# Optimization experiments

Measured on AMD Instinct MI355X. Metric: run time of the kernel, lower is better.

## Reference

```python
import jax, jax.numpy as jnp
import numpy as np

B, L, D, H, DH, M = 2, 2048, 512, 8, 2048, 128  # batch, seq, d_model, heads, d_hidden, max_rel_pos
HD = D // H
EPS = 1e-5


def _ln(x, w, b):
    mu = jnp.mean(x, axis=-1, keepdims=True)
    var = jnp.mean((x - mu) ** 2, axis=-1, keepdims=True)
    return (x - mu) * jax.lax.rsqrt(var + EPS) * w + b


def setup_inputs() -> dict:
    key = jax.random.key(0)
    ks = jax.random.split(key, 8)
    s = 0.02  # init std for weights
    return {
        "x": jax.random.normal(ks[0], (B, L, D), jnp.float32),
        "ln1_w": jnp.ones((D,), jnp.float32),
        "ln1_b": jnp.zeros((D,), jnp.float32),
        "qkv_w": jax.random.normal(ks[1], (D, 3 * D), jnp.float32) * s,
        "qkv_b": jnp.zeros((3 * D,), jnp.float32),
        "out_w": jax.random.normal(ks[2], (D, D), jnp.float32) * s,
        "out_b": jnp.zeros((D,), jnp.float32),
        "rel_bias": jax.random.normal(ks[3], (H, 2 * M - 1), jnp.float32) * s,
        "gamma1": 1e-4 * jnp.ones((D,), jnp.float32),
        "ln2_w": jnp.ones((D,), jnp.float32),
        "ln2_b": jnp.zeros((D,), jnp.float32),
        "ffn_in_w": jax.random.normal(ks[4], (D, 2 * DH), jnp.float32) * s,
        "ffn_in_b": jnp.zeros((2 * DH,), jnp.float32),
        "ffn_out_w": jax.random.normal(ks[5], (DH, D), jnp.float32) * s,
        "ffn_out_b": jnp.zeros((D,), jnp.float32),
        "gamma2": 1e-4 * jnp.ones((D,), jnp.float32),
    }


def _forward(x, ln1_w, ln1_b, qkv_w, qkv_b, out_w, out_b, rel_bias, gamma1,
             ln2_w, ln2_b, ffn_in_w, ffn_in_b, ffn_out_w, ffn_out_b, gamma2):
    b, l, d = x.shape
    # --- PreNorm attention with T5-style relative position bias ---
    h = _ln(x, ln1_w, ln1_b)
    qkv = h @ qkv_w + qkv_b                           # [B, L, 3D]
    q, k, v = jnp.split(qkv, 3, axis=-1)
    q = q.reshape(b, l, H, HD)
    k = k.reshape(b, l, H, HD)
    v = v.reshape(b, l, H, HD)
    scale = 1.0 / jnp.sqrt(jnp.asarray(HD, x.dtype))
    scores = jnp.einsum("bqhd,bkhd->bhqk", q, k) * scale   # [B, H, L, L]
    # relative position bias: clip(i - j) indexed into learned table
    ctx = jnp.arange(l)[:, None] - jnp.arange(l)[None, :]
    ctx = jnp.clip(ctx, -(M - 1), M - 1) + (M - 1)          # [L, L] in [0, 2M-2]
    rel = rel_bias[:, ctx]                                  # [H, L, L]
    scores = scores + rel[None]
    attn = jax.nn.softmax(scores, axis=-1)
    o = jnp.einsum("bhqk,bkhd->bqhd", attn, v).reshape(b, l, d)
    o = o @ out_w + out_b
    x = x + o * gamma1                                      # LayerScale residual
    # --- PreNorm GEGLU FFN ---
    h2 = _ln(x, ln2_w, ln2_b)
    ab = h2 @ ffn_in_w + ffn_in_b                           # [B, L, 2*DH]
    a, bgate = jnp.split(ab, 2, axis=-1)
    f = jax.nn.gelu(bgate, approximate=False) * a
    f = f @ ffn_out_w + ffn_out_b
    x = x + f * gamma2
    return x, attn


def reference(x, ln1_w, ln1_b, qkv_w, qkv_b, out_w, out_b, rel_bias, gamma1,
              ln2_w, ln2_b, ffn_in_w, ffn_in_b, ffn_out_w, ffn_out_b, gamma2):
    return _forward(x, ln1_w, ln1_b, qkv_w, qkv_b, out_w, out_b, rel_bias, gamma1,
                    ln2_w, ln2_b, ffn_in_w, ffn_in_b, ffn_out_w, ffn_out_b, gamma2)
```

## Files before the change

### kernel.cpp

```cpp
#include <hip/hip_runtime.h>
#include <math.h>

typedef __attribute__((ext_vector_type(4))) float f32x4;
typedef __attribute__((ext_vector_type(8))) short bf16x8;
typedef __attribute__((ext_vector_type(4))) short s16x4;

#if __has_builtin(__builtin_amdgcn_exp2f)
#define EXP2(x) __builtin_amdgcn_exp2f(x)
#else
#define EXP2(x) exp2f(x)
#endif

__device__ __forceinline__ unsigned short f2bf(float f) {
  union { float f; unsigned u; } v; v.f = f;
  return (unsigned short)((v.u + 0x7fffu + ((v.u >> 16) & 1u)) >> 16);
}

__global__ void ln_kernel(const float* __restrict__ in, const float* __restrict__ w,
                          const float* __restrict__ b, unsigned short* __restrict__ out) {
  __shared__ float sh[4];
  const int t = threadIdx.x;
  const float* p = in + (size_t)blockIdx.x * 512;
  float a0 = p[t], a1 = p[t + 256];
  float s = a0 + a1;
#pragma unroll
  for (int o = 32; o; o >>= 1) s += __shfl_down(s, o);
  if ((t & 63) == 0) sh[t >> 6] = s;
  __syncthreads();
  s = sh[0] + sh[1] + sh[2] + sh[3];
  float mu = s * (1.0f / 512.0f);
  float d0 = a0 - mu, d1 = a1 - mu;
  float q = d0 * d0 + d1 * d1;
  __syncthreads();
#pragma unroll
  for (int o = 32; o; o >>= 1) q += __shfl_down(q, o);
  if ((t & 63) == 0) sh[t >> 6] = q;
  __syncthreads();
  q = sh[0] + sh[1] + sh[2] + sh[3];
  float rstd = rsqrtf(q * (1.0f / 512.0f) + 1e-5f);
  unsigned short* po = out + (size_t)blockIdx.x * 512;
  po[t]       = f2bf(d0 * rstd * w[t] + b[t]);
  po[t + 256] = f2bf(d1 * rstd * w[t + 256] + b[t + 256]);
}

__global__ void transpose_w(const float* __restrict__ in, unsigned short* __restrict__ out,
                            int ldi, int ldo, long ibs, long obs) {
  __shared__ float tile[32][33];
  const float* ip = in + (long)blockIdx.z * ibs;
  unsigned short* op = out + (long)blockIdx.z * obs;
  const int tx = threadIdx.x & 31;
  const int ty = threadIdx.x >> 5;
  const int n0 = blockIdx.x * 32, k0 = blockIdx.y * 32;
#pragma unroll
  for (int i = 0; i < 4; ++i)
    tile[ty + i * 8][tx] = ip[(size_t)(k0 + ty + i * 8) * ldi + n0 + tx];
  __syncthreads();
#pragma unroll
  for (int i = 0; i < 4; ++i)
    op[(size_t)(n0 + ty + i * 8) * ldo + k0 + tx] = f2bf(tile[tx][ty + i * 8]);
}

template <int WM, int WN, int TM, int TN, int EPI>
__global__ __launch_bounds__(256) void gemm_bb(
    const unsigned short* __restrict__ A, const unsigned short* __restrict__ Bt,
    float* __restrict__ C, unsigned short* __restrict__ Cbf,
    int K, int lda, int ldb, int ldc,
    const float* __restrict__ bias, const float* __restrict__ resid,
    const float* __restrict__ gamma) {
  constexpr int BM = WM * TM * 16;
  constexpr int BN = WN * TN * 16;
  __shared__ short As[BM * 32];
  __shared__ short Bs[BN * 32];

  const int tid = threadIdx.x;
  const int m0 = blockIdx.y * BM, n0 = blockIdx.x * BN;
  const int w = tid >> 6, lane = tid & 63;
  const int wm = w / WN, wn = w % WN;
  const int lrow = lane & 15, lq = lane >> 4;

  f32x4 acc[TM][TN];
#pragma unroll
  for (int i = 0; i < TM; ++i)
#pragma unroll
    for (int j = 0; j < TN; ++j) acc[i][j] = (f32x4){0.f, 0.f, 0.f, 0.f};

  for (int k0 = 0; k0 < K; k0 += 32) {
    __syncthreads();
#pragma unroll
    for (int it = 0; it < BM / 64; ++it) {
      int c = it * 256 + tid;
      int row = c >> 2, col = (c & 3) << 3;
      *(bf16x8*)(As + row * 32 + col) =
          *(const bf16x8*)(A + (size_t)(m0 + row) * lda + k0 + col);
    }
#pragma unroll
    for (int it = 0; it < BN / 64; ++it) {
      int c = it * 256 + tid;
      int row = c >> 2, col = (c & 3) << 3;
      *(bf16x8*)(Bs + row * 32 + col) =
          *(const bf16x8*)(Bt + (size_t)(n0 + row) * ldb + k0 + col);
    }
    __syncthreads();

    bf16x8 af[TM], bf[TN];
#pragma unroll
    for (int mi = 0; mi < TM; ++mi)
      af[mi] = *(const bf16x8*)(As + (wm * TM * 16 + mi * 16 + lrow) * 32 + lq * 8);
#pragma unroll
    for (int nj = 0; nj < TN; ++nj)
      bf[nj] = *(const bf16x8*)(Bs + (wn * TN * 16 + nj * 16 + lrow) * 32 + lq * 8);
#pragma unroll
    for (int mi = 0; mi < TM; ++mi)
#pragma unroll
      for (int nj = 0; nj < TN; ++nj)
        acc[mi][nj] = __builtin_amdgcn_mfma_f32_16x16x32_bf16(af[mi], bf[nj], acc[mi][nj], 0, 0, 0);
  }

#pragma unroll
  for (int mi = 0; mi < TM; ++mi) {
#pragma unroll
    for (int nj = 0; nj < TN; ++nj) {
      int gm0 = m0 + wm * TM * 16 + mi * 16 + lq * 4;
      int gn = n0 + wn * TN * 16 + nj * 16 + lrow;
#pragma unroll
      for (int r = 0; r < 4; ++r) {
        int gm = gm0 + r;
        size_t idx = (size_t)gm * ldc + gn;
        float v = acc[mi][nj][r];
        if constexpr (EPI == 0) {
          C[idx] = v + bias[gn];
        } else if constexpr (EPI == 4) {
          float u = v + bias[gn];
          if (gn < 1024)
            Cbf[idx] = f2bf(gn < 512 ? u * 0.18033688011112042f : u);
          else
            C[idx] = u;
        } else {
          C[idx] = resid[idx] + (v + bias[gn]) * gamma[gn];
        }
      }
    }
  }
}

__global__ __launch_bounds__(256) void ffn1_gate_kernel(
    const unsigned short* __restrict__ A, const unsigned short* __restrict__ Bt,
    unsigned short* __restrict__ F, const float* __restrict__ bias) {
  __shared__ short As[128 * 32];
  __shared__ short Bs[64 * 32];
  __shared__ short Bs2[64 * 32];

  const int tid = threadIdx.x;
  const int n0 = blockIdx.x * 64, m0 = blockIdx.y * 128;
  const int w = tid >> 6, lane = tid & 63;
  const int wm = w >> 1, wn = w & 1;
  const int lrow = lane & 15, lq = lane >> 4;

  f32x4 acca[4][2], accb[4][2];
#pragma unroll
  for (int i = 0; i < 4; ++i)
#pragma unroll
    for (int j = 0; j < 2; ++j) {
      acca[i][j] = (f32x4){0.f, 0.f, 0.f, 0.f};
      accb[i][j] = (f32x4){0.f, 0.f, 0.f, 0.f};
    }

  for (int k0 = 0; k0 < 512; k0 += 32) {
    __syncthreads();
#pragma unroll
    for (int it = 0; it < 2; ++it) {
      int c = it * 256 + tid;
      int row = c >> 2, col = (c & 3) << 3;
      *(bf16x8*)(As + row * 32 + col) =
          *(const bf16x8*)(A + (size_t)(m0 + row) * 512 + k0 + col);
    }
    {
      int c = tid;
      int row = c >> 2, col = (c & 3) << 3;
      *(bf16x8*)(Bs + row * 32 + col) =
          *(const bf16x8*)(Bt + (size_t)(n0 + row) * 512 + k0 + col);
      *(bf16x8*)(Bs2 + row * 32 + col) =
          *(const bf16x8*)(Bt + (size_t)(2048 + n0 + row) * 512 + k0 + col);
    }
    __syncthreads();

    bf16x8 af[4], ba[2], bb[2];
#pragma unroll
    for (int mi = 0; mi < 4; ++mi)
      af[mi] = *(const bf16x8*)(As + (wm * 64 + mi * 16 + lrow) * 32 + lq * 8);
#pragma unroll
    for (int nj = 0; nj < 2; ++nj) {
      ba[nj] = *(const bf16x8*)(Bs + (wn * 32 + nj * 16 + lrow) * 32 + lq * 8);
      bb[nj] = *(const bf16x8*)(Bs2 + (wn * 32 + nj * 16 + lrow) * 32 + lq * 8);
    }
#pragma unroll
    for (int mi = 0; mi < 4; ++mi)
#pragma unroll
      for (int nj = 0; nj < 2; ++nj) {
        acca[mi][nj] = __builtin_amdgcn_mfma_f32_16x16x32_bf16(af[mi], ba[nj], acca[mi][nj], 0, 0, 0);
        accb[mi][nj] = __builtin_amdgcn_mfma_f32_16x16x32_bf16(af[mi], bb[nj], accb[mi][nj], 0, 0, 0);
      }
  }

#pragma unroll
  for (int mi = 0; mi < 4; ++mi)
#pragma unroll
    for (int nj = 0; nj < 2; ++nj) {
      int gm0 = m0 + wm * 64 + mi * 16 + lq * 4;
      int gn = n0 + wn * 32 + nj * 16 + lrow;
#pragma unroll
      for (int r = 0; r < 4; ++r) {
        float a = acca[mi][nj][r] + bias[gn];
        float bg = accb[mi][nj][r] + bias[2048 + gn];
        float g = 0.5f * bg * (1.0f + erff(bg * 0.70710678118654752f));
        F[(size_t)(gm0 + r) * 2048 + gn] = f2bf(g * a);
      }
    }
}

__global__ __launch_bounds__(256, 4) void attn_fused(
    const unsigned short* __restrict__ qkvbf, const unsigned short* __restrict__ vt,
    const float* __restrict__ rel, float* __restrict__ attn, unsigned short* __restrict__ o) {
  __shared__ __align__(16) float p_f32[4 * 16 * 64];
  __shared__ float erel[256];
  __shared__ float rsum[32];
  __shared__ float rinv[32];

  const int tid = threadIdx.x;
  const int flat = blockIdx.y * 64 + blockIdx.x;
  const int swz = (flat & 7) * 128 + (flat >> 3);
  const int bh = swz >> 6;
  const int m0 = (swz & 63) * 32;
  const int b = bh >> 3, h = bh & 7;

  const int w = tid >> 6, lane = tid & 63;
  const int wm = w >> 1, wn = w & 1;
  const int lrow = lane & 15, lq = lane >> 4;

  const unsigned short* qb = qkvbf + (size_t)(b * 2048) * 1536 + h * 64;
  const unsigned short* kb = qb + 512;
  const unsigned short* vb = vt + (size_t)bh * 64 * 2048;
  float* ab = attn + (size_t)bh * 2048 * 2048;
  const float* relh = rel + h * 255;

  if (tid < 32) rsum[tid] = 0.f;
  if (tid < 255) erel[tid] = __expf(relh[tid]);

  bf16x8 qf[2];
#pragma unroll
  for (int c = 0; c < 2; ++c)
    qf[c] = *(const bf16x8*)(qb + (size_t)(m0 + wm * 16 + lrow) * 1536 + c * 32 + lq * 8);

  const unsigned short* krow = kb + (size_t)(wn * 64 + lrow) * 1536 + lq * 8;
  const unsigned short* vrow = vb + (size_t)lrow * 2048 + wn * 64 + lq * 8;

  __syncthreads();

  float psum[4] = {0.f, 0.f, 0.f, 0.f};
  const int dbase = (m0 + wm * 16 + lq * 4) - (wn * 64 + lrow);
  for (int t = 0; t < 16; ++t) {
    const int kt0 = t * 128;
    f32x4 acc[4];
#pragma unroll
    for (int nj = 0; nj < 4; ++nj) acc[nj] = (f32x4){0.f, 0.f, 0.f, 0.f};
#pragma unroll
    for (int c = 0; c < 2; ++c) {
      bf16x8 kf[4];
#pragma unroll
      for (int nj = 0; nj < 4; ++nj)
        kf[nj] = *(const bf16x8*)(krow + (size_t)(kt0 + nj * 16) * 1536 + c * 32);
#pragma unroll
      for (int nj = 0; nj < 4; ++nj)
        acc[nj] = __builtin_amdgcn_mfma_f32_16x16x32_bf16(qf[c], kf[nj], acc[nj], 0, 0, 0);
    }
    const int Dt = m0 - kt0;
    if (Dt >= 256 || Dt <= -160) {
      float ec = erel[Dt >= 256 ? 254 : 0];
#pragma unroll
      for (int r = 0; r < 4; ++r) {
        float s = 0.f;
#pragma unroll
        for (int nj = 0; nj < 4; ++nj) s += EXP2(acc[nj][r]);
        psum[r] += ec * s;
      }
    } else {
#pragma unroll
      for (int nj = 0; nj < 4; ++nj) {
        int d0 = dbase - kt0 - nj * 16;
#pragma unroll
        for (int r = 0; r < 4; ++r) {
          int d = d0 + r;
          d = d < -127 ? -127 : (d > 127 ? 127 : d);
          psum[r] += EXP2(acc[nj][r]) * erel[d + 127];
        }
      }
    }
  }
#pragma unroll
  for (int off = 1; off < 16; off <<= 1)
#pragma unroll
    for (int r = 0; r < 4; ++r) psum[r] += __shfl_xor(psum[r], off);
  if (lrow == 0) {
#pragma unroll
    for (int r = 0; r < 4; ++r) atomicAdd(&rsum[wm * 16 + lq * 4 + r], psum[r]);
  }
  __syncthreads();
  if (tid < 32) rinv[tid] = 1.0f / rsum[tid];
  __syncthreads();
  float rv[4];
#pragma unroll
  for (int r = 0; r < 4; ++r) rv[r] = rinv[wm * 16 + lq * 4 + r];

  f32x4 oacc[4];
#pragma unroll
  for (int nj = 0; nj < 4; ++nj) oacc[nj] = (f32x4){0.f, 0.f, 0.f, 0.f};
  float* pw = p_f32 + w * (16 * 64);

  const int wsw = lq << 4;
  const int rsw = ((lrow >> 2) & 3) << 4;

  for (int t = 0; t < 16; ++t) {
    const int kt0 = t * 128;
    f32x4 acc[4];
#pragma unroll
    for (int nj = 0; nj < 4; ++nj) acc[nj] = (f32x4){0.f, 0.f, 0.f, 0.f};
#pragma unroll
    for (int c = 0; c < 2; ++c) {
      bf16x8 kf[4];
#pragma unroll
      for (int nj = 0; nj < 4; ++nj)
        kf[nj] = *(const bf16x8*)(krow + (size_t)(kt0 + nj * 16) * 1536 + c * 32);
#pragma unroll
      for (int nj = 0; nj < 4; ++nj)
        acc[nj] = __builtin_amdgcn_mfma_f32_16x16x32_bf16(qf[c], kf[nj], acc[nj], 0, 0, 0);
    }

    const int Dt = m0 - kt0;
    if (Dt >= 256 || Dt <= -160) {
      float ec = erel[Dt >= 256 ? 254 : 0];
#pragma unroll
      for (int r = 0; r < 4; ++r) {
        float fr = ec * rv[r];
        int prow = lq * 4 + r;
#pragma unroll
        for (int nj = 0; nj < 4; ++nj) {
          float e = EXP2(acc[nj][r]) * fr;
          pw[prow * 64 + ((nj * 16 + lrow) ^ wsw)] = e;
        }
      }
    } else {
#pragma unroll
      for (int r = 0; r < 4; ++r) {
        int prow = lq * 4 + r;
        int d0 = dbase - kt0 + r;
#pragma unroll
        for (int nj = 0; nj < 4; ++nj) {
          int d = d0 - nj * 16;
          d = d < -127 ? -127 : (d > 127 ? 127 : d);
          float e = EXP2(acc[nj][r]) * (erel[d + 127] * rv[r]);
          pw[prow * 64 + ((nj * 16 + lrow) ^ wsw)] = e;
        }
      }
    }

#pragma unroll
    for (int it = 0; it < 4; ++it) {
      int rr = lq * 4 + it;
      f32x4 vv = *(const f32x4*)(pw + rr * 64 + ((lrow * 4) ^ wsw));
      __builtin_nontemporal_store(
          vv, (f32x4*)(ab + (size_t)(m0 + wm * 16 + rr) * 2048 + kt0 + wn * 64 + lrow * 4));
    }

#pragma unroll
    for (int c2 = 0; c2 < 2; ++c2) {
      const float* pp = pw + lrow * 64 + ((c2 * 32 + lq * 8) ^ rsw);
      f32x4 pa = *(const f32x4*)pp;
      f32x4 pb = *(const f32x4*)(pp + 4);
      bf16x8 ap = {(short)f2bf(pa[0]), (short)f2bf(pa[1]), (short)f2bf(pa[2]), (short)f2bf(pa[3]),
                   (short)f2bf(pb[0]), (short)f2bf(pb[1]), (short)f2bf(pb[2]), (short)f2bf(pb[3])};
      bf16x8 bv[4];
#pragma unroll
      for (int nj = 0; nj < 4; ++nj)
        bv[nj] = *(const bf16x8*)(vrow + (size_t)(nj * 16) * 2048 + kt0 + c2 * 32);
#pragma unroll
      for (int nj = 0; nj < 4; ++nj)
        oacc[nj] = __builtin_amdgcn_mfma_f32_16x16x32_bf16(ap, bv[nj], oacc[nj], 0, 0, 0);
    }
  }

  __syncthreads();
  float* osc = p_f32;
  if (wn == 0) {
#pragma unroll
    for (int nj = 0; nj < 4; ++nj)
#pragma unroll
      for (int r = 0; r < 4; ++r)
        osc[(wm * 16 + lq * 4 + r) * 64 + nj * 16 + lrow] = oacc[nj][r];
  }
  __syncthreads();
  if (wn == 1) {
#pragma unroll
    for (int nj = 0; nj < 4; ++nj)
#pragma unroll
      for (int r = 0; r < 4; ++r) {
        int rr = m0 + wm * 16 + lq * 4 + r;
        float v = oacc[nj][r] + osc[(wm * 16 + lq * 4 + r) * 64 + nj * 16 + lrow];
        o[(size_t)(b * 2048 + rr) * 512 + h * 64 + nj * 16 + lrow] = f2bf(v);
      }
  }
}

extern "C" void kernel_launch(void* const* d_in, const int* in_sizes, int n_in,
                              void* d_out, int out_size, void* d_ws, size_t ws_size,
                              hipStream_t stream) {
  (void)in_sizes; (void)n_in; (void)out_size; (void)ws_size;
  const float* x        = (const float*)d_in[0];
  const float* ln1_w    = (const float*)d_in[1];
  const float* ln1_b    = (const float*)d_in[2];
  const float* qkv_w    = (const float*)d_in[3];
  const float* qkv_b    = (const float*)d_in[4];
  const float* out_w    = (const float*)d_in[5];
  const float* out_b    = (const float*)d_in[6];
  const float* rel_bias = (const float*)d_in[7];
  const float* gamma1   = (const float*)d_in[8];
  const float* ln2_w    = (const float*)d_in[9];
  const float* ln2_b    = (const float*)d_in[10];
  const float* ffn_in_w = (const float*)d_in[11];
  const float* ffn_in_b = (const float*)d_in[12];
  const float* ffn_out_w  = (const float*)d_in[13];
  const float* ffn_out_b  = (const float*)d_in[14];
  const float* gamma2   = (const float*)d_in[15];

  float* x_out = (float*)d_out;
  float* attn  = x_out + (size_t)2 * 2048 * 512;

  float* ws  = (float*)d_ws;
  float* qkv = ws;
  float* x1  = qkv + 6291456;
  unsigned short* h_bf  = (unsigned short*)(x1 + 2097152);
  unsigned short* o_bf  = h_bf + 2097152;
  unsigned short* f_bf  = o_bf + 2097152;
  unsigned short* qkvbf = f_bf;
  unsigned short* bt_qkv  = f_bf + 8388608;
  unsigned short* bt_out  = bt_qkv + 786432;
  unsigned short* bt_ffn1 = bt_out + 262144;
  unsigned short* bt_ffn2 = bt_ffn1 + 2097152;
  unsigned short* vt      = bt_ffn2 + 1048576;

  transpose_w<<<dim3(48, 16, 1), 256, 0, stream>>>(qkv_w,     bt_qkv,  1536, 512,  0, 0);
  transpose_w<<<dim3(16, 16, 1), 256, 0, stream>>>(out_w,     bt_out,  512,  512,  0, 0);
  transpose_w<<<dim3(128, 16, 1), 256, 0, stream>>>(ffn_in_w, bt_ffn1, 4096, 512,  0, 0);
  transpose_w<<<dim3(16, 64, 1), 256, 0, stream>>>(ffn_out_w, bt_ffn2, 512,  2048, 0, 0);

  ln_kernel<<<4096, 256, 0, stream>>>(x, ln1_w, ln1_b, h_bf);

  gemm_bb<2, 2, 4, 2, 4><<<dim3(24, 32, 1), 256, 0, stream>>>(
      h_bf, bt_qkv, qkv, qkvbf, 512, 512, 512, 1536, qkv_b, nullptr, nullptr);

  transpose_w<<<dim3(2, 64, 8), 256, 0, stream>>>(
      qkv + 1024, vt, 1536, 2048, 64, (long)64 * 2048);
  transpose_w<<<dim3(2, 64, 8), 256, 0, stream>>>(
      qkv + (size_t)2048 * 1536 + 1024, vt + (size_t)8 * 64 * 2048, 1536, 2048, 64,
      (long)64 * 2048);

  attn_fused<<<dim3(64, 16, 1), 256, 0, stream>>>(qkvbf, vt, rel_bias, attn, o_bf);

  gemm_bb<2, 2, 4, 2, 3><<<dim3(8, 32, 1), 256, 0, stream>>>(
      o_bf, bt_out, x1, nullptr, 512, 512, 512, 512, out_b, x, gamma1);

  ln_kernel<<<4096, 256, 0, stream>>>(x1, ln2_w, ln2_b, h_bf);

  ffn1_gate_kernel<<<dim3(32, 32, 1), 256, 0, stream>>>(h_bf, bt_ffn1, f_bf, ffn_in_b);

  gemm_bb<2, 2, 4, 2, 3><<<dim3(8, 32, 1), 256, 0, stream>>>(
      f_bf, bt_ffn2, x_out, nullptr, 2048, 2048, 2048, 512, ffn_out_b, x1, gamma2);
}
```

Before: 572.1 us.

## Fuse V transpose into QKV GEMM, shrink attention tile, deepen GEMM K-step

The QKV GEMM epilogue now writes V straight to the transposed bf16 layout, which removes the fp32 qkv buffer and the two V transpose launches. The four weight transposes become a single launch. The GEMM and FFN1 kernels step K by 64 with padded LDS rows to cut syncs and bank conflicts. The out-proj and FFN2 GEMMs use smaller M tiles for more blocks. Attention now uses 16-row query tiles with four waves splitting keys and higher occupancy, at the cost of re-reading K/V more often and an extra cross-wave reduction.

After: 583.7 us. +2.0%, slower.

```diff
diff --git a/kernel.cpp b/kernel.cpp
--- a/kernel.cpp
+++ b/kernel.cpp
@@ -43,34 +43,41 @@
   po[t + 256] = f2bf(d1 * rstd * w[t + 256] + b[t + 256]);
 }
 
-__global__ void transpose_w(const float* __restrict__ in, unsigned short* __restrict__ out,
-                            int ldi, int ldo, long ibs, long obs) {
+__global__ void transpose_all(const float* __restrict__ w0, unsigned short* __restrict__ o0,
+                              const float* __restrict__ w1, unsigned short* __restrict__ o1,
+                              const float* __restrict__ w2, unsigned short* __restrict__ o2,
+                              const float* __restrict__ w3, unsigned short* __restrict__ o3) {
   __shared__ float tile[32][33];
-  const float* ip = in + (long)blockIdx.z * ibs;
-  unsigned short* op = out + (long)blockIdx.z * obs;
+  int idx = blockIdx.x;
+  const float* in; unsigned short* out; int ldi, ldo, nx;
+  if (idx < 768)        { in = w0; out = o0; ldi = 1536; ldo = 512;  nx = 48; }
+  else if (idx < 1024)  { idx -= 768;  in = w1; out = o1; ldi = 512;  ldo = 512;  nx = 16; }
+  else if (idx < 3072)  { idx -= 1024; in = w2; out = o2; ldi = 4096; ldo = 512;  nx = 128; }
+  else                  { idx -= 3072; in = w3; out = o3; ldi = 512;  ldo = 2048; nx = 16; }
   const int tx = threadIdx.x & 31;
   const int ty = threadIdx.x >> 5;
-  const int n0 = blockIdx.x * 32, k0 = blockIdx.y * 32;
+  const int n0 = (idx % nx) * 32, k0 = (idx / nx) * 32;
 #pragma unroll
   for (int i = 0; i < 4; ++i)
-    tile[ty + i * 8][tx] = ip[(size_t)(k0 + ty + i * 8) * ldi + n0 + tx];
+    tile[ty + i * 8][tx] = in[(size_t)(k0 + ty + i * 8) * ldi + n0 + tx];
   __syncthreads();
 #pragma unroll
   for (int i = 0; i < 4; ++i)
-    op[(size_t)(n0 + ty + i * 8) * ldo + k0 + tx] = f2bf(tile[tx][ty + i * 8]);
+    out[(size_t)(n0 + ty + i * 8) * ldo + k0 + tx] = f2bf(tile[tx][ty + i * 8]);
 }
 
 template <int WM, int WN, int TM, int TN, int EPI>
 __global__ __launch_bounds__(256) void gemm_bb(
     const unsigned short* __restrict__ A, const unsigned short* __restrict__ Bt,
-    float* __restrict__ C, unsigned short* __restrict__ Cbf,
+    float* __restrict__ C, unsigned short* __restrict__ Cbf, unsigned short* __restrict__ Vt,
     int K, int lda, int ldb, int ldc,
     const float* __restrict__ bias, const float* __restrict__ resid,
     const float* __restrict__ gamma) {
   constexpr int BM = WM * TM * 16;
   constexpr int BN = WN * TN * 16;
-  __shared__ short As[BM * 32];
-  __shared__ short Bs[BN * 32];
+  constexpr int LDS_STRIDE = 72;
+  __shared__ short As[BM * LDS_STRIDE];
+  __shared__ short Bs[BN * LDS_STRIDE];
 
   const int tid = threadIdx.x;
   const int m0 = blockIdx.y * BM, n0 = blockIdx.x * BN;
@@ -84,36 +91,42 @@
 #pragma unroll
     for (int j = 0; j < TN; ++j) acc[i][j] = (f32x4){0.f, 0.f, 0.f, 0.f};
 
-  for (int k0 = 0; k0 < K; k0 += 32) {
+  for (int k0 = 0; k0 < K; k0 += 64) {
     __syncthreads();
 #pragma unroll
-    for (int it = 0; it < BM / 64; ++it) {
+    for (int it = 0; it < BM / 32; ++it) {
       int c = it * 256 + tid;
-      int row = c >> 2, col = (c & 3) << 3;
-      *(bf16x8*)(As + row * 32 + col) =
+      int row = c >> 3, col = (c & 7) << 3;
+      *(bf16x8*)(As + row * LDS_STRIDE + col) =
           *(const bf16x8*)(A + (size_t)(m0 + row) * lda + k0 + col);
     }
 #pragma unroll
-    for (int it = 0; it < BN / 64; ++it) {
+    for (int it = 0; it < BN / 32; ++it) {
       int c = it * 256 + tid;
-      int row = c >> 2, col = (c & 3) << 3;
-      *(bf16x8*)(Bs + row * 32 + col) =
+      int row = c >> 3, col = (c & 7) << 3;
+      *(bf16x8*)(Bs + row * LDS_STRIDE + col) =
           *(const bf16x8*)(Bt + (size_t)(n0 + row) * ldb + k0 + col);
     }
     __syncthreads();
 
-    bf16x8 af[TM], bf[TN];
+    bf16x8 af[TM][2], bf[TN][2];
 #pragma unroll
     for (int mi = 0; mi < TM; ++mi)
-      af[mi] = *(const bf16x8*)(As + (wm * TM * 16 + mi * 16 + lrow) * 32 + lq * 8);
+#pragma unroll
+      for (int c = 0; c < 2; ++c)
+        af[mi][c] = *(const bf16x8*)(As + (wm * TM * 16 + mi * 16 + lrow) * LDS_STRIDE + c * 32 + lq * 8);
 #pragma unroll
     for (int nj = 0; nj < TN; ++nj)
-      bf[nj] = *(const bf16x8*)(Bs + (wn * TN * 16 + nj * 16 + lrow) * 32 + lq * 8);
+#pragma unroll
+      for (int c = 0; c < 2; ++c)
+        bf[nj][c] = *(const bf16x8*)(Bs + (wn * TN * 16 + nj * 16 + lrow) * LDS_STRIDE + c * 32 + lq * 8);
 #pragma unroll
     for (int mi = 0; mi < TM; ++mi)
 #pragma unroll
       for (int nj = 0; nj < TN; ++nj)
-        acc[mi][nj] = __builtin_amdgcn_mfma_f32_16x16x32_bf16(af[mi], bf[nj], acc[mi][nj], 0, 0, 0);
+#pragma unroll
+        for (int c = 0; c < 2; ++c)
+          acc[mi][nj] = __builtin_amdgcn_mfma_f32_16x16x32_bf16(af[mi][c], bf[nj][c], acc[mi][nj], 0, 0, 0);
   }
 
 #pragma unroll
@@ -122,6 +135,17 @@
     for (int nj = 0; nj < TN; ++nj) {
       int gm0 = m0 + wm * TM * 16 + mi * 16 + lq * 4;
       int gn = n0 + wn * TN * 16 + nj * 16 + lrow;
+      if constexpr (EPI == 4) {
+        if (gn >= 1024) {
+          int h = (gn - 1024) >> 6, dd = (gn - 1024) & 63;
+          int bb = gm0 >> 11, l0 = gm0 & 2047;
+          float bs = bias[gn];
+          s16x4 r4 = {(short)f2bf(acc[mi][nj][0] + bs), (short)f2bf(acc[mi][nj][1] + bs),
+                      (short)f2bf(acc[mi][nj][2] + bs), (short)f2bf(acc[mi][nj][3] + bs)};
+          *(s16x4*)(Vt + ((size_t)(bb * 8 + h) * 64 + dd) * 2048 + l0) = r4;
+          continue;
+        }
+      }
 #pragma unroll
       for (int r = 0; r < 4; ++r) {
         int gm = gm0 + r;
@@ -131,10 +155,7 @@
           C[idx] = v + bias[gn];
         } else if constexpr (EPI == 4) {
           float u = v + bias[gn];
-          if (gn < 1024)
-            Cbf[idx] = f2bf(gn < 512 ? u * 0.18033688011112042f : u);
-          else
-            C[idx] = u;
+          Cbf[idx] = f2bf(gn < 512 ? u * 0.18033688011112042f : u);
         } else {
           C[idx] = resid[idx] + (v + bias[gn]) * gamma[gn];
         }
@@ -146,9 +167,10 @@
 __global__ __launch_bounds__(256) void ffn1_gate_kernel(
     const unsigned short* __restrict__ A, const unsigned short* __restrict__ Bt,
     unsigned short* __restrict__ F, const float* __restrict__ bias) {
-  __shared__ short As[128 * 32];
-  __shared__ short Bs[64 * 32];
-  __shared__ short Bs2[64 * 32];
+  constexpr int LDS_STRIDE = 72;
+  __shared__ short As[128 * LDS_STRIDE];
+  __shared__ short Bs[64 * LDS_STRIDE];
+  __shared__ short Bs2[64 * LDS_STRIDE];
 
   const int tid = threadIdx.x;
   const int n0 = blockIdx.x * 64, m0 = blockIdx.y * 128;
@@ -165,41 +187,48 @@
       accb[i][j] = (f32x4){0.f, 0.f, 0.f, 0.f};
     }
 
-  for (int k0 = 0; k0 < 512; k0 += 32) {
+  for (int k0 = 0; k0 < 512; k0 += 64) {
     __syncthreads();
+#pragma unroll
+    for (int it = 0; it < 4; ++it) {
+      int c = it * 256 + tid;
+      int row = c >> 3, col = (c & 7) << 3;
+      *(bf16x8*)(As + row * LDS_STRIDE + col) =
+          *(const bf16x8*)(A + (size_t)(m0 + row) * 512 + k0 + col);
+    }
 #pragma unroll
     for (int it = 0; it < 2; ++it) {
       int c = it * 256 + tid;
-      int row = c >> 2, col = (c & 3) << 3;
-      *(bf16x8*)(As + row * 32 + col) =
-          *(const bf16x8*)(A + (size_t)(m0 + row) * 512 + k0 + col);
-    }
-    {
-      int c = tid;
-      int row = c >> 2, col = (c & 3) << 3;
-      *(bf16x8*)(Bs + row * 32 + col) =
+      int row = c >> 3, col = (c & 7) << 3;
+      *(bf16x8*)(Bs + row * LDS_STRIDE + col) =
           *(const bf16x8*)(Bt + (size_t)(n0 + row) * 512 + k0 + col);
-      *(bf16x8*)(Bs2 + row * 32 + col) =
+      *(bf16x8*)(Bs2 + row * LDS_STRIDE + col) =
           *(const bf16x8*)(Bt + (size_t)(2048 + n0 + row) * 512 + k0 + col);
     }
     __syncthreads();
 
-    bf16x8 af[4], ba[2], bb[2];
+    bf16x8 af[4][2], ba[2][2], bb[2][2];
 #pragma unroll
     for (int mi = 0; mi < 4; ++mi)
-      af[mi] = *(const bf16x8*)(As + (wm * 64 + mi * 16 + lrow) * 32 + lq * 8);
-#pragma unroll
-    for (int nj = 0; nj < 2; ++nj) {
-      ba[nj] = *(const bf16x8*)(Bs + (wn * 32 + nj * 16 + lrow) * 32 + lq * 8);
-      bb[nj] = *(const bf16x8*)(Bs2 + (wn * 32 + nj * 16 + lrow) * 32 + lq * 8);
-    }
+#pragma unroll
+      for (int c = 0; c < 2; ++c)
+        af[mi][c] = *(const bf16x8*)(As + (wm * 64 + mi * 16 + lrow) * LDS_STRIDE + c * 32 + lq * 8);
+#pragma unroll
+    for (int nj = 0; nj < 2; ++nj)
+#pragma unroll
+      for (int c = 0; c < 2; ++c) {
+        ba[nj][c] = *(const bf16x8*)(Bs + (wn * 32 + nj * 16 + lrow) * LDS_STRIDE + c * 32 + lq * 8);
+        bb[nj][c] = *(const bf16x8*)(Bs2 + (wn * 32 + nj * 16 + lrow) * LDS_STRIDE + c * 32 + lq * 8);
+      }
 #pragma unroll
     for (int mi = 0; mi < 4; ++mi)
 #pragma unroll
-      for (int nj = 0; nj < 2; ++nj) {
-        acca[mi][nj] = __builtin_amdgcn_mfma_f32_16x16x32_bf16(af[mi], ba[nj], acca[mi][nj], 0, 0, 0);
-        accb[mi][nj] = __builtin_amdgcn_mfma_f32_16x16x32_bf16(af[mi], bb[nj], accb[mi][nj], 0, 0, 0);
-      }
+      for (int nj = 0; nj < 2; ++nj)
+#pragma unroll
+        for (int c = 0; c < 2; ++c) {
+          acca[mi][nj] = __builtin_amdgcn_mfma_f32_16x16x32_bf16(af[mi][c], ba[nj][c], acca[mi][nj], 0, 0, 0);
+          accb[mi][nj] = __builtin_amdgcn_mfma_f32_16x16x32_bf16(af[mi][c], bb[nj][c], accb[mi][nj], 0, 0, 0);
+        }
   }
 
 #pragma unroll
@@ -218,23 +247,22 @@
     }
 }
 
-__global__ __launch_bounds__(256, 4) void attn_fused(
+__global__ __launch_bounds__(256, 8) void attn_fused(
     const unsigned short* __restrict__ qkvbf, const unsigned short* __restrict__ vt,
     const float* __restrict__ rel, float* __restrict__ attn, unsigned short* __restrict__ o) {
-  __shared__ __align__(16) float p_f32[4 * 16 * 64];
+  __shared__ __align__(16) float scr[3072];
   __shared__ float erel[256];
-  __shared__ float rsum[32];
-  __shared__ float rinv[32];
+  __shared__ float rsum[16];
+  __shared__ float rinv[16];
 
   const int tid = threadIdx.x;
-  const int flat = blockIdx.y * 64 + blockIdx.x;
-  const int swz = (flat & 7) * 128 + (flat >> 3);
-  const int bh = swz >> 6;
-  const int m0 = (swz & 63) * 32;
+  const int flat = blockIdx.y * 128 + blockIdx.x;
+  const int swz = (flat & 7) * 256 + (flat >> 3);
+  const int bh = swz >> 7;
+  const int m0 = (swz & 127) * 16;
   const int b = bh >> 3, h = bh & 7;
 
   const int w = tid >> 6, lane = tid & 63;
-  const int wm = w >> 1, wn = w & 1;
   const int lrow = lane & 15, lq = lane >> 4;
 
   const unsigned short* qb = qkvbf + (size_t)(b * 2048) * 1536 + h * 64;
@@ -243,49 +271,45 @@
   float* ab = attn + (size_t)bh * 2048 * 2048;
   const float* relh = rel + h * 255;
 
-  if (tid < 32) rsum[tid] = 0.f;
+  if (tid < 16) rsum[tid] = 0.f;
   if (tid < 255) erel[tid] = __expf(relh[tid]);
 
   bf16x8 qf[2];
 #pragma unroll
   for (int c = 0; c < 2; ++c)
-    qf[c] = *(const bf16x8*)(qb + (size_t)(m0 + wm * 16 + lrow) * 1536 + c * 32 + lq * 8);
-
-  const unsigned short* krow = kb + (size_t)(wn * 64 + lrow) * 1536 + lq * 8;
-  const unsigned short* vrow = vb + (size_t)lrow * 2048 + wn * 64 + lq * 8;
+    qf[c] = *(const bf16x8*)(qb + (size_t)(m0 + lrow) * 1536 + c * 32 + lq * 8);
+
+  const unsigned short* krow = kb + (size_t)(w * 32 + lrow) * 1536 + lq * 8;
+  const unsigned short* vrow = vb + (size_t)lrow * 2048 + w * 32 + lq * 8;
 
   __syncthreads();
 
   float psum[4] = {0.f, 0.f, 0.f, 0.f};
-  const int dbase = (m0 + wm * 16 + lq * 4) - (wn * 64 + lrow);
+  const int dbase = (m0 + lq * 4) - (w * 32 + lrow);
   for (int t = 0; t < 16; ++t) {
     const int kt0 = t * 128;
-    f32x4 acc[4];
-#pragma unroll
-    for (int nj = 0; nj < 4; ++nj) acc[nj] = (f32x4){0.f, 0.f, 0.f, 0.f};
+    f32x4 acc[2];
+#pragma unroll
+    for (int nj = 0; nj < 2; ++nj) acc[nj] = (f32x4){0.f, 0.f, 0.f, 0.f};
 #pragma unroll
     for (int c = 0; c < 2; ++c) {
-      bf16x8 kf[4];
-#pragma unroll
-      for (int nj = 0; nj < 4; ++nj)
+      bf16x8 kf[2];
+#pragma unroll
+      for (int nj = 0; nj < 2; ++nj)
         kf[nj] = *(const bf16x8*)(krow + (size_t)(kt0 + nj * 16) * 1536 + c * 32);
 #pragma unroll
-      for (int nj = 0; nj < 4; ++nj)
+      for (int nj = 0; nj < 2; ++nj)
         acc[nj] = __builtin_amdgcn_mfma_f32_16x16x32_bf16(qf[c], kf[nj], acc[nj], 0, 0, 0);
     }
     const int Dt = m0 - kt0;
-    if (Dt >= 256 || Dt <= -160) {
-      float ec = erel[Dt >= 256 ? 254 : 0];
-#pragma unroll
-      for (int r = 0; r < 4; ++r) {
-        float s = 0.f;
-#pragma unroll
-        for (int nj = 0; nj < 4; ++nj) s += EXP2(acc[nj][r]);
-        psum[r] += ec * s;
-      }
+    if (Dt >= 254 || Dt <= -144) {
+      float ec = erel[Dt >= 254 ? 254 : 0];
+#pragma unroll
+      for (int r = 0; r < 4; ++r)
+        psum[r] += ec * (EXP2(acc[0][r]) + EXP2(acc[1][r]));
     } else {
 #pragma unroll
-      for (int nj = 0; nj < 4; ++nj) {
+      for (int nj = 0; nj < 2; ++nj) {
         int d0 = dbase - kt0 - nj * 16;
 #pragma unroll
         for (int r = 0; r < 4; ++r) {
@@ -302,51 +326,48 @@
     for (int r = 0; r < 4; ++r) psum[r] += __shfl_xor(psum[r], off);
   if (lrow == 0) {
 #pragma unroll
-    for (int r = 0; r < 4; ++r) atomicAdd(&rsum[wm * 16 + lq * 4 + r], psum[r]);
-  }
-  __syncthreads();
-  if (tid < 32) rinv[tid] = 1.0f / rsum[tid];
+    for (int r = 0; r < 4; ++r) atomicAdd(&rsum[lq * 4 + r], psum[r]);
+  }
+  __syncthreads();
+  if (tid < 16) rinv[tid] = 1.0f / rsum[tid];
   __syncthreads();
   float rv[4];
 #pragma unroll
-  for (int r = 0; r < 4; ++r) rv[r] = rinv[wm * 16 + lq * 4 + r];
+  for (int r = 0; r < 4; ++r) rv[r] = rinv[lq * 4 + r];
 
   f32x4 oacc[4];
 #pragma unroll
   for (int nj = 0; nj < 4; ++nj) oacc[nj] = (f32x4){0.f, 0.f, 0.f, 0.f};
-  float* pw = p_f32 + w * (16 * 64);
-
-  const int wsw = lq << 4;
-  const int rsw = ((lrow >> 2) & 3) << 4;
+  float* pw = scr + w * 512;
+  const int wsw = lq << 3;
+  const int rsw = ((lrow >> 2) & 3) << 3;
 
   for (int t = 0; t < 16; ++t) {
     const int kt0 = t * 128;
-    f32x4 acc[4];
-#pragma unroll
-    for (int nj = 0; nj < 4; ++nj) acc[nj] = (f32x4){0.f, 0.f, 0.f, 0.f};
+    f32x4 acc[2];
+#pragma unroll
+    for (int nj = 0; nj < 2; ++nj) acc[nj] = (f32x4){0.f, 0.f, 0.f, 0.f};
 #pragma unroll
     for (int c = 0; c < 2; ++c) {
-      bf16x8 kf[4];
-#pragma unroll
-      for (int nj = 0; nj < 4; ++nj)
+      bf16x8 kf[2];
+#pragma unroll
+      for (int nj = 0; nj < 2; ++nj)
         kf[nj] = *(const bf16x8*)(krow + (size_t)(kt0 + nj * 16) * 1536 + c * 32);
 #pragma unroll
-      for (int nj = 0; nj < 4; ++nj)
+      for (int nj = 0; nj < 2; ++nj)
         acc[nj] = __builtin_amdgcn_mfma_f32_16x16x32_bf16(qf[c], kf[nj], acc[nj], 0, 0, 0);
     }
 
     const int Dt = m0 - kt0;
-    if (Dt >= 256 || Dt <= -160) {
-      float ec = erel[Dt >= 256 ? 254 : 0];
+    if (Dt >= 254 || Dt <= -144) {
+      float ec = erel[Dt >= 254 ? 254 : 0];
 #pragma unroll
       for (int r = 0; r < 4; ++r) {
         float fr = ec * rv[r];
         int prow = lq * 4 + r;
 #pragma unroll
-        for (int nj = 0; nj < 4; ++nj) {
-          float e = EXP2(acc[nj][r]) * fr;
-          pw[prow * 64 + ((nj * 16 + lrow) ^ wsw)] = e;
-        }
+        for (int nj = 0; nj < 2; ++nj)
+          pw[prow * 32 + ((nj * 16 + lrow) ^ wsw)] = EXP2(acc[nj][r]) * fr;
       }
     } else {
 #pragma unroll
@@ -354,26 +375,25 @@
         int prow = lq * 4 + r;
         int d0 = dbase - kt0 + r;
 #pragma unroll
-        for (int nj = 0; nj < 4; ++nj) {
+        for (int nj = 0; nj < 2; ++nj) {
           int d = d0 - nj * 16;
           d = d < -127 ? -127 : (d > 127 ? 127 : d);
-          float e = EXP2(acc[nj][r]) * (erel[d + 127] * rv[r]);
-          pw[prow * 64 + ((nj * 16 + lrow) ^ wsw)] = e;
+          pw[prow * 32 + ((nj * 16 + lrow) ^ wsw)] = EXP2(acc[nj][r]) * (erel[d + 127] * rv[r]);
         }
       }
     }
 
 #pragma unroll
-    for (int it = 0; it < 4; ++it) {
-      int rr = lq * 4 + it;
-      f32x4 vv = *(const f32x4*)(pw + rr * 64 + ((lrow * 4) ^ wsw));
+    for (int it = 0; it < 2; ++it) {
+      int unit = it * 64 + lane;
+      int row = unit >> 3, cg = unit & 7;
+      f32x4 vv = *(const f32x4*)(pw + row * 32 + ((cg * 4) ^ (((row >> 2) & 3) << 3)));
       __builtin_nontemporal_store(
-          vv, (f32x4*)(ab + (size_t)(m0 + wm * 16 + rr) * 2048 + kt0 + wn * 64 + lrow * 4));
-    }
-
-#pragma unroll
-    for (int c2 = 0; c2 < 2; ++c2) {
-      const float* pp = pw + lrow * 64 + ((c2 * 32 + lq * 8) ^ rsw);
+          vv, (f32x4*)(ab + (size_t)(m0 + row) * 2048 + kt0 + w * 32 + cg * 4));
+    }
+
+    {
+      const float* pp = pw + lrow * 32 + ((lq * 8) ^ rsw);
       f32x4 pa = *(const f32x4*)pp;
       f32x4 pb = *(const f32x4*)(pp + 4);
       bf16x8 ap = {(short)f2bf(pa[0]), (short)f2bf(pa[1]), (short)f2bf(pa[2]), (short)f2bf(pa[3]),
@@ -381,7 +401,7 @@
       bf16x8 bv[4];
 #pragma unroll
       for (int nj = 0; nj < 4; ++nj)
-        bv[nj] = *(const bf16x8*)(vrow + (size_t)(nj * 16) * 2048 + kt0 + c2 * 32);
+        bv[nj] = *(const bf16x8*)(vrow + (size_t)(nj * 16) * 2048 + kt0);
 #pragma unroll
       for (int nj = 0; nj < 4; ++nj)
         oacc[nj] = __builtin_amdgcn_mfma_f32_16x16x32_bf16(ap, bv[nj], oacc[nj], 0, 0, 0);
@@ -389,23 +409,22 @@
   }
 
   __syncthreads();
-  float* osc = p_f32;
-  if (wn == 0) {
+  if (w > 0) {
 #pragma unroll
     for (int nj = 0; nj < 4; ++nj)
 #pragma unroll
       for (int r = 0; r < 4; ++r)
-        osc[(wm * 16 + lq * 4 + r) * 64 + nj * 16 + lrow] = oacc[nj][r];
-  }
-  __syncthreads();
-  if (wn == 1) {
+        scr[(w - 1) * 1024 + (lq * 4 + r) * 64 + nj * 16 + lrow] = oacc[nj][r];
+  }
+  __syncthreads();
+  if (w == 0) {
 #pragma unroll
     for (int nj = 0; nj < 4; ++nj)
 #pragma unroll
       for (int r = 0; r < 4; ++r) {
-        int rr = m0 + wm * 16 + lq * 4 + r;
-        float v = oacc[nj][r] + osc[(wm * 16 + lq * 4 + r) * 64 + nj * 16 + lrow];
-        o[(size_t)(b * 2048 + rr) * 512 + h * 64 + nj * 16 + lrow] = f2bf(v);
+        int ii = (lq * 4 + r) * 64 + nj * 16 + lrow;
+        float v = oacc[nj][r] + scr[ii] + scr[1024 + ii] + scr[2048 + ii];
+        o[(size_t)(b * 2048 + m0 + lq * 4 + r) * 512 + h * 64 + nj * 16 + lrow] = f2bf(v);
       }
   }
 }
@@ -435,8 +454,7 @@
   float* attn  = x_out + (size_t)2 * 2048 * 512;
 
   float* ws  = (float*)d_ws;
-  float* qkv = ws;
-  float* x1  = qkv + 6291456;
+  float* x1  = ws;
   unsigned short* h_bf  = (unsigned short*)(x1 + 2097152);
   unsigned short* o_bf  = h_bf + 2097152;
   unsigned short* f_bf  = o_bf + 2097152;
@@ -447,31 +465,23 @@
   unsigned short* bt_ffn2 = bt_ffn1 + 2097152;
   unsigned short* vt      = bt_ffn2 + 1048576;
 
-  transpose_w<<<dim3(48, 16, 1), 256, 0, stream>>>(qkv_w,     bt_qkv,  1536, 512,  0, 0);
-  transpose_w<<<dim3(16, 16, 1), 256, 0, stream>>>(out_w,     bt_out,  512,  512,  0, 0);
-  transpose_w<<<dim3(128, 16, 1), 256, 0, stream>>>(ffn_in_w, bt_ffn1, 4096, 512,  0, 0);
-  transpose_w<<<dim3(16, 64, 1), 256, 0, stream>>>(ffn_out_w, bt_ffn2, 512,  2048, 0, 0);
+  transpose_all<<<4096, 256, 0, stream>>>(qkv_w, bt_qkv, out_w, bt_out,
+                                          ffn_in_w, bt_ffn1, ffn_out_w, bt_ffn2);
 
   ln_kernel<<<4096, 256, 0, stream>>>(x, ln1_w, ln1_b, h_bf);
 
   gemm_bb<2, 2, 4, 2, 4><<<dim3(24, 32, 1), 256, 0, stream>>>(
-      h_bf, bt_qkv, qkv, qkvbf, 512, 512, 512, 1536, qkv_b, nullptr, nullptr);
-
-  transpose_w<<<dim3(2, 64, 8), 256, 0, stream>>>(
-      qkv + 1024, vt, 1536, 2048, 64, (long)64 * 2048);
-  transpose_w<<<dim3(2, 64, 8), 256, 0, stream>>>(
-      qkv + (size_t)2048 * 1536 + 1024, vt + (size_t)8 * 64 * 2048, 1536, 2048, 64,
-      (long)64 * 2048);
-
-  attn_fused<<<dim3(64, 16, 1), 256, 0, stream>>>(qkvbf, vt, rel_bias, attn, o_bf);
-
-  gemm_bb<2, 2, 4, 2, 3><<<dim3(8, 32, 1), 256, 0, stream>>>(
-      o_bf, bt_out, x1, nullptr, 512, 512, 512, 512, out_b, x, gamma1);
+      h_bf, bt_qkv, nullptr, qkvbf, vt, 512, 512, 512, 1536, qkv_b, nullptr, nullptr);
+
+  attn_fused<<<dim3(128, 16, 1), 256, 0, stream>>>(qkvbf, vt, rel_bias, attn, o_bf);
+
+  gemm_bb<2, 2, 2, 2, 3><<<dim3(8, 64, 1), 256, 0, stream>>>(
+      o_bf, bt_out, x1, nullptr, nullptr, 512, 512, 512, 512, out_b, x, gamma1);
 
   ln_kernel<<<4096, 256, 0, stream>>>(x1, ln2_w, ln2_b, h_bf);
 
   ffn1_gate_kernel<<<dim3(32, 32, 1), 256, 0, stream>>>(h_bf, bt_ffn1, f_bf, ffn_in_b);
 
-  gemm_bb<2, 2, 4, 2, 3><<<dim3(8, 32, 1), 256, 0, stream>>>(
-      f_bf, bt_ffn2, x_out, nullptr, 2048, 2048, 2048, 512, ffn_out_b, x1, gamma2);
-}
+  gemm_bb<2, 2, 2, 2, 3><<<dim3(8, 64, 1), 256, 0, stream>>>(
+      f_bf, bt_ffn2, x_out, nullptr, nullptr, 2048, 2048, 2048, 512, ffn_out_b, x1, gamma2);
+}
```
